# Kernel optimization log

Hardware: AMD Instinct MI355X
Metric: run time of the kernel (lower is better)

The kernel has to match this reference:

```python
import jax, jax.numpy as jnp
import numpy as np

# ---- static configuration (matches init_kwargs / input_specs) ----
B, N = 4, 128            # images, proposals per image
C = 256                  # feature channels (in_channels)
HF, WF = 23, 30          # feature map size (input 736x960 / 32)
PH, PW = 7, 7            # pooled_size
SCALE = 1.0 / 32.0       # scale_factor
HIMG, WIMG = HF * 32, WF * 32
KH = HF // PH + 2        # max rows any pooling bin can span
KW = WF // PW + 2        # max cols any pooling bin can span
HID, OUT = 256, 5
NEG = -1e30


def _roi_pool_one(f, box):
    """Quantized ROI max pooling for one proposal.
    f: (C, HF, WF) feature map; box: (4,) [x1,y1,x2,y2] in feature coords.
    Returns (C, PH, PW)."""
    box = jax.lax.stop_gradient(box)  # indices are non-differentiable
    x1 = jnp.clip(jnp.floor(box[0]).astype(jnp.int32), 0, WF - 1)
    y1 = jnp.clip(jnp.floor(box[1]).astype(jnp.int32), 0, HF - 1)
    roi_w = jnp.clip(jnp.ceil(box[2]).astype(jnp.int32) - x1, 1, WF)
    roi_h = jnp.clip(jnp.ceil(box[3]).astype(jnp.int32) - y1, 1, HF)
    ph = jnp.arange(PH)
    pw = jnp.arange(PW)
    hs = y1 + (ph * roi_h) // PH                       # bin row starts (PH,)
    he = y1 + ((ph + 1) * roi_h + PH - 1) // PH        # bin row ends (ceil)
    ws = x1 + (pw * roi_w) // PW
    we = x1 + ((pw + 1) * roi_w + PW - 1) // PW
    hidx = hs[:, None] + jnp.arange(KH)[None, :]       # (PH, KH)
    hval = (hidx < he[:, None]) & (hidx < HF)
    widx = ws[:, None] + jnp.arange(KW)[None, :]       # (PW, KW)
    wval = (widx < we[:, None]) & (widx < WF)
    rows = f[:, jnp.clip(hidx, 0, HF - 1), :]          # (C, PH, KH, WF) gather
    rmax = jnp.max(jnp.where(hval[None, :, :, None], rows, NEG), axis=2)  # (C, PH, WF)
    cols = rmax[:, :, jnp.clip(widx, 0, WF - 1)]       # (C, PH, PW, KW) gather
    return jnp.max(jnp.where(wval[None, None], cols, NEG), axis=3)        # (C, PH, PW)


# vmap over proposals, then over images: (B,C,HF,WF),(B,N,4) -> (B,N,C,PH,PW)
_roi_pool = jax.vmap(jax.vmap(_roi_pool_one, in_axes=(None, 0)), in_axes=(0, 0))


def setup_inputs() -> dict:
    key = jax.random.key(0)
    ks = jax.random.split(key, 8)
    features = jax.random.normal(ks[0], (B, C, HF, WF), jnp.float32)
    # valid proposals in image coordinates (min box side ~32 px)
    x1 = jax.random.uniform(ks[1], (B, N)) * (WIMG - 32.0)
    y1 = jax.random.uniform(ks[2], (B, N)) * (HIMG - 32.0)
    x2 = x1 + 32.0 + jax.random.uniform(ks[3], (B, N)) * (WIMG - 32.0 - x1)
    y2 = y1 + 32.0 + jax.random.uniform(ks[4], (B, N)) * (HIMG - 32.0 - y1)
    conf = jax.random.normal(ks[5], (B, N))
    proposals = jnp.stack([x1, y1, x2, y2, conf], axis=-1)  # (B, N, 5)
    W1 = jax.random.normal(ks[6], (HID, C * PH * PW), jnp.float32) * 0.01
    b1 = jnp.zeros((HID,), jnp.float32)
    W2 = jax.random.normal(ks[7], (OUT, HID), jnp.float32) * 0.01
    b2 = jnp.zeros((OUT,), jnp.float32)
    return {"features": features, "proposals": proposals,
            "W1": W1, "b1": b1, "W2": W2, "b2": b2}


def reference(features, proposals, W1, b1, W2, b2):
    boxes_feat = proposals[..., :4] * SCALE                 # image -> feature coords
    pooled = _roi_pool(features, boxes_feat)                # (B, N, C, PH, PW)
    flat = pooled.reshape(B, N, C * PH * PW)
    h = jax.nn.relu(jnp.einsum('bnf,hf->bnh', flat, W1) + b1)
    out = jnp.einsum('bnh,oh->bno', h, W2) + b2             # (B, N, 5)
    refined_boxes = proposals[..., :4] + out[..., :4]
    refined_conf = jax.nn.sigmoid(proposals[..., 4:5] + out[..., 4:5])
    return jnp.concatenate([refined_boxes, refined_conf], axis=-1)  # (B, N, 5)
```

## Files before the change

### kernel.cpp

```cpp
#include <hip/hip_runtime.h>
#include <math.h>

#define Bq 4
#define Nq 128
#define Cq 256
#define HFq 23
#define WFq 30
#define PHq 7
#define PWq 7
#define HIDq 256
#define OUTq 5
#define Fq (Cq*PHq*PWq)
#define Mq (Bq*Nq)
#define HWq (HFq*WFq)
#define SCALEq (1.0f/32.0f)
#define NEGq (-1e30f)
#define KHq 5
#define KWq 6
#define SPLITK 14
#define KCH (Fq/SPLITK)
#define BKq 64
#define KSTEPS (KCH/BKq)

typedef float f32x4 __attribute__((ext_vector_type(4)));
typedef __bf16 bf16x8 __attribute__((ext_vector_type(8)));
typedef unsigned short u16x8 __attribute__((ext_vector_type(8)));

__device__ __forceinline__ unsigned short f2b(float f) {
    unsigned int u = __float_as_uint(f);
    unsigned int r = (u + 0x7FFFu + ((u >> 16) & 1u)) >> 16;
    return (unsigned short)r;
}

__global__ __launch_bounds__(256) void k_prep(const float* __restrict__ feat,
                                              unsigned short* __restrict__ ft,
                                              const float* __restrict__ W1,
                                              unsigned short* __restrict__ w1p,
                                              float* __restrict__ h) {
    __shared__ __align__(16) unsigned short smem[Fq];
    int bid = blockIdx.x;
    int tid = threadIdx.x;
    if (bid < 704) {
        float (*t)[33] = (float (*)[33])smem;
        int bb  = bid / 176;
        int rem = bid % 176;
        int x0 = (rem % 22) * 32;
        int c0 = (rem / 22) * 32;
        int tx = tid & 31, ty = tid >> 5;
        const float* src = feat + (size_t)bb * Cq * HWq;
        unsigned short* dst = ft + (size_t)bb * HWq * Cq;
#pragma unroll
        for (int i = 0; i < 4; ++i) {
            int c = c0 + ty + i * 8;
            int x = x0 + tx;
            if (x < HWq) t[ty + i * 8][tx] = src[(size_t)c * HWq + x];
        }
        __syncthreads();
        int u = tid & 15, xl = tid >> 4;
#pragma unroll
        for (int i = 0; i < 2; ++i) {
            int xloc = xl + i * 16;
            int x = x0 + xloc;
            if (x < HWq) {
                ushort2 o;
                o.x = f2b(t[u * 2][xloc]);
                o.y = f2b(t[u * 2 + 1][xloc]);
                *(ushort2*)(dst + (size_t)x * Cq + c0 + u * 2) = o;
            }
        }
    } else if (bid < 960) {
        int j = bid - 704;
        const float4* src = (const float4*)(W1 + (size_t)j * Fq);
        for (int i = tid; i < Fq / 4; i += 256) {
            float4 v = src[i];
            ushort4 o;
            o.x = f2b(v.x); o.y = f2b(v.y); o.z = f2b(v.z); o.w = f2b(v.w);
            ((ushort4*)smem)[i] = o;
        }
        __syncthreads();
        uint4* dst = (uint4*)(w1p + (size_t)j * Fq);
        for (int i = tid; i < Fq / 8; i += 256) {
            int base = i * 8;
            int cell = base >> 8;
            int c0v = base & 255;
            unsigned short tmp[8];
#pragma unroll
            for (int u2 = 0; u2 < 8; ++u2) tmp[u2] = smem[(c0v + u2) * 49 + cell];
            dst[i] = *(const uint4*)tmp;
        }
    } else {
        f32x4* h4 = (f32x4*)h;
        int base = (bid - 960) * 4096;
        f32x4 z = {0.f, 0.f, 0.f, 0.f};
#pragma unroll
        for (int u2 = 0; u2 < 16; ++u2) h4[base + u2 * 256 + tid] = z;
    }
}

__global__ __launch_bounds__(256) void k_pool(const unsigned short* __restrict__ ft,
                                              const float* __restrict__ props,
                                              unsigned short* __restrict__ pooled) {
    int wave = threadIdx.x >> 6;
    int lane = threadIdx.x & 63;
    int half = lane >> 5;
    int cl = lane & 31;
    int cell = blockIdx.y * 4 + wave;
    if (cell >= PHq * PWq) return;
    int m = blockIdx.x;
    int b = m >> 7;
    const float* pr = props + (size_t)m * 5;
    float b0 = pr[0] * SCALEq, b1v = pr[1] * SCALEq;
    float b2v = pr[2] * SCALEq, b3v = pr[3] * SCALEq;
    int x1 = min(max((int)floorf(b0), 0), WFq - 1);
    int y1 = min(max((int)floorf(b1v), 0), HFq - 1);
    int rw = min(max((int)ceilf(b2v) - x1, 1), WFq);
    int rh = min(max((int)ceilf(b3v) - y1, 1), HFq);
    const unsigned short* ftb = ft + (size_t)b * HWq * Cq + cl * 8;
    unsigned short* pm = pooled + (size_t)m * Fq + cl * 8;

    int ph = cell / 7;
    int pw = cell - ph * 7;
    int hs = y1 + (ph * rh) / PHq;
    int he = min(y1 + ((ph + 1) * rh + PHq - 1) / PHq, HFq);
    int ws = x1 + (pw * rw) / PWq;
    int we = min(x1 + ((pw + 1) * rw + PWq - 1) / PWq, WFq);
    float acc[8];
#pragma unroll
    for (int u = 0; u < 8; ++u) acc[u] = NEGq;
#pragma unroll
    for (int kh = 0; kh < KHq; ++kh) {
        if (hs + kh < he) {
            const unsigned short* rowp = ftb + (size_t)((hs + kh) * WFq) * Cq;
#pragma unroll
            for (int kw2 = 0; kw2 < 3; ++kw2) {
                int w = ws + kw2 * 2 + half;
                if (w < we) {
                    u16x8 v = *(const u16x8*)(rowp + (size_t)w * Cq);
#pragma unroll
                    for (int u = 0; u < 8; ++u)
                        acc[u] = fmaxf(acc[u], __uint_as_float((unsigned)v[u] << 16));
                }
            }
        }
    }
#pragma unroll
    for (int u = 0; u < 8; ++u) acc[u] = fmaxf(acc[u], __shfl_xor(acc[u], 32));
    if (half == 0) {
        u16x8 o;
#pragma unroll
        for (int u = 0; u < 8; ++u) o[u] = f2b(acc[u]);
        *(u16x8*)(pm + (size_t)cell * Cq) = o;
    }
}

__global__ __launch_bounds__(256) void k_gemm1(const unsigned short* __restrict__ pooled,
                                               const unsigned short* __restrict__ w1p,
                                               float* __restrict__ h) {
    __shared__ __align__(16) unsigned short As[2][64 * BKq];
    __shared__ __align__(16) unsigned short Bs[2][64 * BKq];
    int m0 = blockIdx.x * 64;
    int j0 = blockIdx.y * 64;
    int kz = blockIdx.z;
    int tid = threadIdx.x;
    int r = tid >> 2, qq = tid & 3;
    const uint4* ap = (const uint4*)(pooled + (size_t)(m0 + r) * Fq + (size_t)kz * KCH) + qq;
    const uint4* bp = (const uint4*)(w1p + (size_t)(j0 + r) * Fq + (size_t)kz * KCH) + qq;
    int lane = tid & 63, wv = tid >> 6;
    int q = lane >> 4, mr = lane & 15;
    f32x4 acc0 = {0.f, 0.f, 0.f, 0.f};
    f32x4 acc1 = {0.f, 0.f, 0.f, 0.f};
    f32x4 acc2 = {0.f, 0.f, 0.f, 0.f};
    f32x4 acc3 = {0.f, 0.f, 0.f, 0.f};
    int st1 = r * 8 + ((qq) ^ (r & 7));
    int st2 = r * 8 + ((qq ^ 4) ^ (r & 7));
    int sA = (wv * 16 + mr) * 8;
    int c0k0 = (q) ^ (mr & 7);
    int c0k1 = (q ^ 4) ^ (mr & 7);

    uint4 a0v = ap[0], a1v = ap[4];
    uint4 b0v = bp[0], b1v = bp[4];
    {
        uint4* aw = (uint4*)As[0];
        uint4* bw = (uint4*)Bs[0];
        aw[st1] = a0v; aw[st2] = a1v;
        bw[st1] = b0v; bw[st2] = b1v;
    }
    a0v = ap[8];  a1v = ap[12];
    b0v = bp[8];  b1v = bp[12];
    for (int s = 0; s < KSTEPS; ++s) {
        __syncthreads();
        int cur = s & 1;
        if (s + 1 < KSTEPS) {
            uint4* aw = (uint4*)As[cur ^ 1];
            uint4* bw = (uint4*)Bs[cur ^ 1];
            aw[st1] = a0v; aw[st2] = a1v;
            bw[st1] = b0v; bw[st2] = b1v;
            if (s + 2 < KSTEPS) {
                a0v = ap[(s + 2) * 8];     a1v = ap[(s + 2) * 8 + 4];
                b0v = bp[(s + 2) * 8];     b1v = bp[(s + 2) * 8 + 4];
            }
        }
        const bf16x8* Ab = (const bf16x8*)As[cur];
        const bf16x8* Bb = (const bf16x8*)Bs[cur];
        bf16x8 a0 = Ab[sA + c0k0];
        bf16x8 a1 = Ab[sA + c0k1];
        acc0 = __builtin_amdgcn_mfma_f32_16x16x32_bf16(a0, Bb[(0  + mr) * 8 + c0k0], acc0, 0, 0, 0);
        acc1 = __builtin_amdgcn_mfma_f32_16x16x32_bf16(a0, Bb[(16 + mr) * 8 + c0k0], acc1, 0, 0, 0);
        acc2 = __builtin_amdgcn_mfma_f32_16x16x32_bf16(a0, Bb[(32 + mr) * 8 + c0k0], acc2, 0, 0, 0);
        acc3 = __builtin_amdgcn_mfma_f32_16x16x32_bf16(a0, Bb[(48 + mr) * 8 + c0k0], acc3, 0, 0, 0);
        acc0 = __builtin_amdgcn_mfma_f32_16x16x32_bf16(a1, Bb[(0  + mr) * 8 + c0k1], acc0, 0, 0, 0);
        acc1 = __builtin_amdgcn_mfma_f32_16x16x32_bf16(a1, Bb[(16 + mr) * 8 + c0k1], acc1, 0, 0, 0);
        acc2 = __builtin_amdgcn_mfma_f32_16x16x32_bf16(a1, Bb[(32 + mr) * 8 + c0k1], acc2, 0, 0, 0);
        acc3 = __builtin_amdgcn_mfma_f32_16x16x32_bf16(a1, Bb[(48 + mr) * 8 + c0k1], acc3, 0, 0, 0);
    }
    int mb = m0 + wv * 16 + q * 4;
    int jj = j0 + mr;
#pragma unroll
    for (int r2 = 0; r2 < 4; ++r2) {
        float* row = h + (size_t)(mb + r2) * HIDq + jj;
        atomicAdd(row + 0,  acc0[r2]);
        atomicAdd(row + 16, acc1[r2]);
        atomicAdd(row + 32, acc2[r2]);
        atomicAdd(row + 48, acc3[r2]);
    }
}

__global__ __launch_bounds__(256) void k_tail(const float* __restrict__ h,
                                              const float* __restrict__ b1,
                                              const float* __restrict__ W2,
                                              const float* __restrict__ b2,
                                              const float* __restrict__ props,
                                              float* __restrict__ out) {
    __shared__ float red[OUTq][4];
    int m = blockIdx.x, j = threadIdx.x;
    float hv = fmaxf(h[(size_t)m * HIDq + j] + b1[j], 0.f);
    float p[OUTq];
#pragma unroll
    for (int o = 0; o < OUTq; ++o) p[o] = hv * W2[(size_t)o * HIDq + j];
    int lane = j & 63, wid = j >> 6;
#pragma unroll
    for (int o = 0; o < OUTq; ++o) {
        float v = p[o];
        v += __shfl_xor(v, 1);
        v += __shfl_xor(v, 2);
        v += __shfl_xor(v, 4);
        v += __shfl_xor(v, 8);
        v += __shfl_xor(v, 16);
        v += __shfl_xor(v, 32);
        if (lane == 0) red[o][wid] = v;
    }
    __syncthreads();
    if (j < OUTq) {
        float s = red[j][0] + red[j][1] + red[j][2] + red[j][3] + b2[j];
        float pv = props[(size_t)m * 5 + j];
        float r;
        if (j < 4) r = pv + s;
        else r = 1.f / (1.f + expf(-(pv + s)));
        out[(size_t)m * 5 + j] = r;
    }
}

extern "C" void kernel_launch(void* const* d_in, const int* in_sizes, int n_in,
                              void* d_out, int out_size, void* d_ws, size_t ws_size,
                              hipStream_t stream) {
    const float* feat  = (const float*)d_in[0];
    const float* props = (const float*)d_in[1];
    const float* W1    = (const float*)d_in[2];
    const float* b1    = (const float*)d_in[3];
    const float* W2    = (const float*)d_in[4];
    const float* b2    = (const float*)d_in[5];
    float* out = (float*)d_out;

    char* ws = (char*)d_ws;
    unsigned short* ft     = (unsigned short*)(ws);
    unsigned short* w1p    = (unsigned short*)(ws + 1413120);
    unsigned short* pooled = (unsigned short*)(ws + 7835648);
    float* h               = (float*)(ws + 20680704);

    k_prep<<<968, 256, 0, stream>>>(feat, ft, W1, w1p, h);
    k_pool<<<dim3(Mq, 13), 256, 0, stream>>>(ft, props, pooled);
    k_gemm1<<<dim3(8, 4, SPLITK), 256, 0, stream>>>(pooled, w1p, h);
    k_tail<<<Mq, 256, 0, stream>>>(h, b1, W2, b2, props, out);
}
```

Measured before the change: 109.5 us.

## Fuse MLP tail into split-K GEMM via last-block arrival counter

Removes the separate tail kernel launch by having each GEMM block increment a per-row-tile atomic counter after its split-K atomic adds. The last block to arrive for a 64-row tile computes ReLU, the second linear layer and the box/sigmoid outputs for those rows. This saves one kernel launch and the pass that re-reads h, at the cost of an extra syncthreads and atomic per block and a serialized tail on a few blocks.

```diff
diff --git a/kernel.cpp b/kernel.cpp
--- a/kernel.cpp
+++ b/kernel.cpp
@@ -36,7 +36,8 @@
                                               unsigned short* __restrict__ ft,
                                               const float* __restrict__ W1,
                                               unsigned short* __restrict__ w1p,
-                                              float* __restrict__ h) {
+                                              float* __restrict__ h,
+                                              int* __restrict__ cnt) {
     __shared__ __align__(16) unsigned short smem[Fq];
     int bid = blockIdx.x;
     int tid = threadIdx.x;
@@ -94,6 +95,7 @@
         f32x4 z = {0.f, 0.f, 0.f, 0.f};
 #pragma unroll
         for (int u2 = 0; u2 < 16; ++u2) h4[base + u2 * 256 + tid] = z;
+        if (bid == 960 && tid < Mq / 64) cnt[tid] = 0;
     }
 }
 
@@ -155,9 +157,16 @@
 
 __global__ __launch_bounds__(256) void k_gemm1(const unsigned short* __restrict__ pooled,
                                                const unsigned short* __restrict__ w1p,
-                                               float* __restrict__ h) {
+                                               float* __restrict__ h,
+                                               int* __restrict__ cnt,
+                                               const float* __restrict__ b1,
+                                               const float* __restrict__ W2,
+                                               const float* __restrict__ b2,
+                                               const float* __restrict__ props,
+                                               float* __restrict__ out) {
     __shared__ __align__(16) unsigned short As[2][64 * BKq];
     __shared__ __align__(16) unsigned short Bs[2][64 * BKq];
+    __shared__ int fin;
     int m0 = blockIdx.x * 64;
     int j0 = blockIdx.y * 64;
     int kz = blockIdx.z;
@@ -223,40 +232,55 @@
         atomicAdd(row + 32, acc2[r2]);
         atomicAdd(row + 48, acc3[r2]);
     }
-}
-
-__global__ __launch_bounds__(256) void k_tail(const float* __restrict__ h,
-                                              const float* __restrict__ b1,
-                                              const float* __restrict__ W2,
-                                              const float* __restrict__ b2,
-                                              const float* __restrict__ props,
-                                              float* __restrict__ out) {
-    __shared__ float red[OUTq][4];
-    int m = blockIdx.x, j = threadIdx.x;
-    float hv = fmaxf(h[(size_t)m * HIDq + j] + b1[j], 0.f);
-    float p[OUTq];
-#pragma unroll
-    for (int o = 0; o < OUTq; ++o) p[o] = hv * W2[(size_t)o * HIDq + j];
-    int lane = j & 63, wid = j >> 6;
-#pragma unroll
-    for (int o = 0; o < OUTq; ++o) {
-        float v = p[o];
-        v += __shfl_xor(v, 1);
-        v += __shfl_xor(v, 2);
-        v += __shfl_xor(v, 4);
-        v += __shfl_xor(v, 8);
-        v += __shfl_xor(v, 16);
-        v += __shfl_xor(v, 32);
-        if (lane == 0) red[o][wid] = v;
-    }
     __syncthreads();
-    if (j < OUTq) {
-        float s = red[j][0] + red[j][1] + red[j][2] + red[j][3] + b2[j];
-        float pv = props[(size_t)m * 5 + j];
-        float r;
-        if (j < 4) r = pv + s;
-        else r = 1.f / (1.f + expf(-(pv + s)));
-        out[(size_t)m * 5 + j] = r;
+    if (tid == 0) {
+        int old = __hip_atomic_fetch_add(&cnt[blockIdx.x], 1,
+                                         __ATOMIC_ACQ_REL, __HIP_MEMORY_SCOPE_AGENT);
+        fin = (old == 4 * SPLITK - 1);
+    }
+    __syncthreads();
+    if (!fin) return;
+    int j4 = lane * 4;
+    float b14[4], w2r[OUTq][4];
+#pragma unroll
+    for (int u = 0; u < 4; ++u) b14[u] = b1[j4 + u];
+#pragma unroll
+    for (int o = 0; o < OUTq; ++o)
+#pragma unroll
+        for (int u = 0; u < 4; ++u) w2r[o][u] = W2[(size_t)o * HIDq + j4 + u];
+#pragma unroll
+    for (int rr = 0; rr < 16; ++rr) {
+        int m = m0 + wv * 16 + rr;
+        float hv[4];
+#pragma unroll
+        for (int u = 0; u < 4; ++u) {
+            float hl = __hip_atomic_load(&h[(size_t)m * HIDq + j4 + u],
+                                         __ATOMIC_RELAXED, __HIP_MEMORY_SCOPE_AGENT);
+            hv[u] = fmaxf(hl + b14[u], 0.f);
+        }
+        float s[OUTq];
+#pragma unroll
+        for (int o = 0; o < OUTq; ++o) {
+            float v = hv[0] * w2r[o][0] + hv[1] * w2r[o][1]
+                    + hv[2] * w2r[o][2] + hv[3] * w2r[o][3];
+            v += __shfl_xor(v, 1);
+            v += __shfl_xor(v, 2);
+            v += __shfl_xor(v, 4);
+            v += __shfl_xor(v, 8);
+            v += __shfl_xor(v, 16);
+            v += __shfl_xor(v, 32);
+            s[o] = v;
+        }
+        if (lane < OUTq) {
+            float so = lane == 0 ? s[0] : lane == 1 ? s[1] : lane == 2 ? s[2]
+                     : lane == 3 ? s[3] : s[4];
+            so += b2[lane];
+            float pv = props[(size_t)m * 5 + lane];
+            float rres;
+            if (lane < 4) rres = pv + so;
+            else rres = 1.f / (1.f + expf(-(pv + so)));
+            out[(size_t)m * 5 + lane] = rres;
+        }
     }
 }
 
@@ -276,9 +300,10 @@
     unsigned short* w1p    = (unsigned short*)(ws + 1413120);
     unsigned short* pooled = (unsigned short*)(ws + 7835648);
     float* h               = (float*)(ws + 20680704);
-
-    k_prep<<<968, 256, 0, stream>>>(feat, ft, W1, w1p, h);
+    int* cnt               = (int*)(ws + 21204992);
+
+    k_prep<<<968, 256, 0, stream>>>(feat, ft, W1, w1p, h, cnt);
     k_pool<<<dim3(Mq, 13), 256, 0, stream>>>(ft, props, pooled);
-    k_gemm1<<<dim3(8, 4, SPLITK), 256, 0, stream>>>(pooled, w1p, h);
-    k_tail<<<Mq, 256, 0, stream>>>(h, b1, W2, b2, props, out);
-}
+    k_gemm1<<<dim3(Mq / 64, HIDq / 64, SPLITK), 256, 0, stream>>>(
+        pooled, w1p, h, cnt, b1, W2, b2, props, out);
+}
```

New measurement: 126.1 us. 15.2% more time.
